# Performance work log

Measured on AMD Instinct MI355X. Metric: run time of the kernel, lower is better.

Reference implementation:

```python
import jax, jax.numpy as jnp
import numpy as np

V, E, H, OUT = 100000, 300, 256, 3
B, LS, LT = 128, 128, 8


def _lstm_scan(xs, Wih, Whh, bih, bhh, reverse):
    # xs: [T, B, E] time-major; returns hidden states [T, B, H] in original time order
    h0 = jnp.zeros((xs.shape[1], H), xs.dtype)
    def step(carry, x):
        h, c = carry
        g = x @ Wih.T + bih + h @ Whh.T + bhh  # [B, 4H]
        i, f, gg, o = jnp.split(g, 4, axis=-1)
        c = jax.nn.sigmoid(f) * c + jax.nn.sigmoid(i) * jnp.tanh(gg)
        h = jax.nn.sigmoid(o) * jnp.tanh(c)
        return (h, c), h
    _, hs = jax.lax.scan(step, (h0, h0), xs, reverse=reverse)
    return hs


def _bidir(emb_bte, Wih_f, Whh_f, bih_f, bhh_f, Wih_b, Whh_b, bih_b, bhh_b):
    xs = jnp.transpose(emb_bte, (1, 0, 2))  # [T, B, E]
    hf = _lstm_scan(xs, Wih_f, Whh_f, bih_f, bhh_f, False)
    hb = _lstm_scan(xs, Wih_b, Whh_b, bih_b, bhh_b, True)
    return jnp.transpose(jnp.concatenate([hf, hb], axis=-1), (1, 0, 2))  # [B, T, 2H]


def setup_inputs() -> dict:
    key = jax.random.key(0)
    ks = jax.random.split(key, 32)
    n = lambda i, shape: 0.05 * jax.random.normal(ks[i], shape, dtype=jnp.float32)
    inp = {
        "sentence_source": jax.random.randint(ks[0], (B, LS), 0, V),
        "target_source": jax.random.randint(ks[1], (B, LT), 0, V),
        "emb_W": n(2, (V, E)),
    }
    names = ["sf", "sb", "tf", "tb"]
    for j, nm in enumerate(names):
        base = 3 + 4 * j
        inp[f"Wih_{nm}"] = n(base + 0, (4 * H, E))
        inp[f"Whh_{nm}"] = n(base + 1, (4 * H, H))
        inp[f"bih_{nm}"] = n(base + 2, (4 * H,))
        inp[f"bhh_{nm}"] = n(base + 3, (4 * H,))
    inp["Wout"] = n(20, (OUT, 2 * H))
    inp["bout"] = n(21, (OUT,))
    return inp


def reference(sentence_source, target_source, emb_W,
              Wih_sf, Whh_sf, bih_sf, bhh_sf,
              Wih_sb, Whh_sb, bih_sb, bhh_sb,
              Wih_tf, Whh_tf, bih_tf, bhh_tf,
              Wih_tb, Whh_tb, bih_tb, bhh_tb,
              Wout, bout):
    emb = emb_W.at[0].set(0.0)  # padding_idx=0
    sen = emb[sentence_source]  # [B, LS, E]  (dropout is identity at eval)
    tgt = emb[target_source]    # [B, LT, E]
    sen_h = _bidir(sen, Wih_sf, Whh_sf, bih_sf, bhh_sf, Wih_sb, Whh_sb, bih_sb, bhh_sb)  # [B, LS, 2H]
    tgt_h = _bidir(tgt, Wih_tf, Whh_tf, bih_tf, bhh_tf, Wih_tb, Whh_tb, bih_tb, bhh_tb)  # [B, LT, 2H]
    A = jnp.einsum("bsh,bth->bst", sen_h, tgt_h)          # [B, LS, LT]
    col = jax.nn.softmax(A, axis=1)
    row = jax.nn.softmax(A, axis=2)
    row_vec = jnp.mean(row, axis=1, keepdims=True)         # [B, 1, LT]
    attn = jnp.einsum("bst,bqt->bsq", col, row_vec)        # [B, LS, 1]
    score = jnp.einsum("bsq,bsh->bqh", attn, sen_h)        # [B, 1, 2H]
    logits = score @ Wout.T + bout                         # [B, 1, OUT]
    return jax.nn.softmax(logits, axis=-1).squeeze()       # [B, OUT]
```

## Files before the change

kernel.cpp:

```cpp
#include <hip/hip_runtime.h>


typedef unsigned short u16;
typedef unsigned long long u64;
typedef float f32x4 __attribute__((ext_vector_type(4)));
typedef int   i32x4 __attribute__((ext_vector_type(4)));
typedef short bf16x8 __attribute__((ext_vector_type(8)));
typedef short s16x4 __attribute__((ext_vector_type(4)));
typedef unsigned short u16x4 __attribute__((ext_vector_type(4)));

#define KP 320
#define KPL 328
#define FH 1024
#define HH 256
#define L2E 1.4426950408889634f

struct Ptr4 { const float* p[4]; };

static __device__ __forceinline__ u16 f2bf(float f) {
    unsigned int u = __float_as_uint(f);
    u += 0x7FFFu + ((u >> 16) & 1u);
    return (u16)(u >> 16);
}
static __device__ __forceinline__ float bf2f(u16 s) {
    return __uint_as_float((unsigned int)s << 16);
}
static __device__ __forceinline__ float sigm2(float x) {
    return __builtin_amdgcn_rcpf(1.0f + __builtin_amdgcn_exp2f(-x));
}
static __device__ __forceinline__ float tanh2(float x) {
    return 1.0f - 2.0f * __builtin_amdgcn_rcpf(1.0f + __builtin_amdgcn_exp2f(x));
}
static __device__ __forceinline__ float tanh_(float x) {
    return 1.0f - 2.0f * __builtin_amdgcn_rcpf(1.0f + __expf(2.0f * x));
}

__global__ __launch_bounds__(256) void pre_kernel(
    const int* __restrict__ sen, const int* __restrict__ tgt,
    const float* __restrict__ emb, Ptr4 Wih, Ptr4 Whh, Ptr4 bih, Ptr4 bhh,
    u16* __restrict__ Xs, u16* __restrict__ Xt,
    u16* __restrict__ WihB, float* __restrict__ biasB,
    char* __restrict__ Wq, float* __restrict__ wdq)
{
    int bid = blockIdx.x, tid = threadIdx.x;
    if (bid < 17408) {
        int row = bid;
        int tok; u16* dst;
        if (row < 16384) { tok = sen[row]; dst = Xs + (size_t)row * KP; }
        else             { tok = tgt[row - 16384]; dst = Xt + (size_t)(row - 16384) * KP; }
        const float* src = emb + (size_t)tok * 300;
        for (int k = tid; k < KP; k += 256) {
            float v = (k < 300 && tok != 0) ? src[k] : 0.0f;
            dst[k] = f2bf(v);
        }
    } else if (bid < 22528) {
        int local = bid - 17408;
        int dir = local / 1280, blk = local - dir * 1280;
        int idx = blk * 256 + tid;
        if (idx < FH * KP) {
            int row = idx / KP, k = idx - row * KP;
            float gsc = ((row >> 8) == 2) ? 2.0f * L2E : L2E;
            WihB[(size_t)dir * FH * KP + idx] =
                (k < 300) ? f2bf(Wih.p[dir][row * 300 + k] * gsc) : (u16)0;
        }
        if (idx < FH) {
            float gsc = ((idx >> 8) == 2) ? 2.0f * L2E : L2E;
            biasB[dir * FH + idx] = (bih.p[dir][idx] + bhh.p[dir][idx]) * gsc;
        }
    } else {
        int local = bid - 22528;
        int w = tid >> 6, lane = tid & 63;
        int pair = local * 4 + w;
        int dir = pair >> 10, row = pair & 1023;
        const float* src = Whh.p[dir] + (size_t)row * HH;
        float m = 0.0f;
        for (int k = lane; k < HH; k += 64) m = fmaxf(m, fabsf(src[k]));
        for (int off = 32; off; off >>= 1) m = fmaxf(m, __shfl_down(m, off));
        m = __shfl(m, 0);
        float qs = (m > 0.0f) ? 127.0f / m : 0.0f;
        char* dst = Wq + (size_t)dir * FH * HH + (size_t)row * HH;
        for (int k = lane; k < HH; k += 64) dst[k] = (char)(int)rintf(src[k] * qs);
        if (lane == 0) {
            float gsc = ((row >> 8) == 2) ? 2.0f * L2E : L2E;
            wdq[dir * FH + row] = (m > 0.0f) ? m / (127.0f * 127.0f) * gsc : 0.0f;
        }
    }
}

__global__ __launch_bounds__(256) void input_gemm_kernel(
    const u16* __restrict__ Xs, const u16* __restrict__ Xt,
    const u16* __restrict__ WihB, const float* __restrict__ biasB,
    u16* __restrict__ Gs, u16* __restrict__ Gt)
{
    __shared__ u16 Bs[64][KPL];

    int bid = blockIdx.x;
    const u16* X; const u16* W; const float* bias; u16* G;
    int lbid, nwg, tsh;
    if (bid < 8192) { lbid = bid;        nwg = 8192; tsh = 7;
                      X = Xs; W = WihB;                         bias = biasB;          G = Gs; }
    else            { lbid = bid - 8192; nwg = 512;  tsh = 3;
                      X = Xt; W = WihB + (size_t)2 * FH * KP;   bias = biasB + 2 * FH; G = Gt; }

    int cpx = nwg >> 3;
    int wid = (lbid & 7) * cpx + (lbid >> 3);
    int nblk = wid & 31;
    int mblk = wid >> 5;
    int dirb = nblk >> 4;
    int u0   = (nblk & 15) * 16;
    size_t dirStride = (size_t)(tsh == 7 ? 16384 : 1024) * FH;

    int tid = threadIdx.x;
    int wave = tid >> 6, lane = tid & 63;
    int r = lane & 15, quad = lane >> 4;
    int m0 = mblk * 64 + wave * 16;

#pragma unroll
    for (int it = 0; it < 10; ++it) {
        int idx = it * 256 + tid;
        int row = idx / 40, cc = idx - row * 40;
        int j = row >> 4, rr = row & 15;
        bf16x8 v = *(const bf16x8*)(W + ((size_t)dirb * FH + j * 256 + u0 + rr) * KP + cc * 8);
        *(bf16x8*)&Bs[row][cc * 8] = v;
    }
    __syncthreads();

    const u16* xr = X + (size_t)(m0 + r) * KP + quad * 8;
    f32x4 acc[4] = {};
#pragma unroll
    for (int k0 = 0; k0 < KP; k0 += 32) {
        bf16x8 a = *(const bf16x8*)(xr + k0);
#pragma unroll
        for (int j = 0; j < 4; ++j) {
            bf16x8 b = *(const bf16x8*)&Bs[j * 16 + r][k0 + quad * 8];
            acc[j] = __builtin_amdgcn_mfma_f32_16x16x32_bf16(a, b, acc[j], 0, 0, 0);
        }
    }

#pragma unroll
    for (int reg = 0; reg < 4; ++reg) {
        int m = m0 + quad * 4 + reg;
        int b = m >> tsh, t = m & ((1 << tsh) - 1);
        int unit = u0 + r;
        u16x4 ov;
#pragma unroll
        for (int j = 0; j < 4; ++j)
            ov[j] = f2bf(acc[j][reg] + bias[dirb * FH + j * 256 + unit]);
        *(u16x4*)(G + (size_t)dirb * dirStride + ((size_t)t * 128 + b) * FH + unit * 4) = ov;
    }
}

__global__ __launch_bounds__(1024, 1) void lstm_scan_kernel(
    const char*  __restrict__ WqB,
    const float* __restrict__ wdq,
    const u16*   __restrict__ Gs,
    const u16*   __restrict__ Gt,
    float* __restrict__ senH,
    float* __restrict__ tgtH)
{
    const int bx  = blockIdx.x;
    const int dir = bx >> 3;
    const int b0  = (bx & 7) << 4;
    const int T   = (dir < 2) ? 128 : 8;
    const int rev = dir & 1;

    const char* Wq = WqB + (size_t)dir * FH * HH;
    const u16*  G  = (dir < 2) ? (Gs + (size_t)dir * 16384 * FH)
                               : (Gt + (size_t)(dir - 2) * 1024 * FH);
    float* Hout = (dir < 2) ? senH : tgtH;
    const int hofs = rev ? 256 : 0;

    const int tid  = threadIdx.x;
    const int w    = tid >> 6, lane = tid & 63;
    const int r    = lane & 15, quad = lane >> 4;
    const int u    = w * 16 + r;

    __shared__ __align__(16) char hb8[2][16][272];

    i32x4 Bq[4][4];
    float dqv[4];
#pragma unroll
    for (int g = 0; g < 4; ++g) {
        int row = g * 256 + u;
        dqv[g] = wdq[dir * FH + row];
#pragma unroll
        for (int kt = 0; kt < 4; ++kt)
            Bq[g][kt] = *(const i32x4*)(Wq + ((size_t)row << 8) + kt * 64 + quad * 16);
    }

    for (int i = tid; i < 2 * 16 * 272; i += 1024) (&hb8[0][0][0])[i] = 0;
    __syncthreads();

    float c[4] = {};
    float hreg[4] = {};
    int tprev = 0;

    s16x4 gvA[4], gvB[4];
    {
        const int t0 = rev ? (T - 1) : 0;
#pragma unroll
        for (int reg = 0; reg < 4; ++reg)
            gvA[reg] = *(const s16x4*)(G + ((size_t)t0 * 128 + b0 + quad * 4 + reg) * FH
                                       + u * 4);
    }

    auto body = [&](int cur, s16x4 (&gvU)[4], s16x4 (&gvP)[4],
                    int t, int tn, int doStore) {
#pragma unroll
        for (int reg = 0; reg < 4; ++reg)
            gvP[reg] = *(const s16x4*)(G + ((size_t)tn * 128 + b0 + quad * 4 + reg) * FH
                                       + u * 4);
        if (doStore) {
#pragma unroll
            for (int reg = 0; reg < 4; ++reg)
                Hout[((size_t)(b0 + quad * 4 + reg) * T + tprev) * 512 + hofs + u]
                    = hreg[reg];
        }

        i32x4 acc[4] = {};
#pragma unroll
        for (int kt = 0; kt < 4; ++kt) {
            i32x4 a = *(const i32x4*)&hb8[cur][r][kt * 64 + quad * 16];
#pragma unroll
            for (int g = 0; g < 4; ++g)
                acc[g] = __builtin_amdgcn_mfma_i32_16x16x64_i8(a, Bq[g][kt], acc[g], 0, 0, 0);
        }

#pragma unroll
        for (int reg = 0; reg < 4; ++reg) {
            int bb = quad * 4 + reg;
            float pi = (float)acc[0][reg] * dqv[0] + bf2f((u16)gvU[reg].x);
            float pf = (float)acc[1][reg] * dqv[1] + bf2f((u16)gvU[reg].y);
            float pg = (float)acc[2][reg] * dqv[2] + bf2f((u16)gvU[reg].z);
            float po = (float)acc[3][reg] * dqv[3] + bf2f((u16)gvU[reg].w);
            float ig = sigm2(pi), fg = sigm2(pf), gg = tanh2(pg), og = sigm2(po);
            float cn = fg * c[reg] + ig * gg;
            c[reg] = cn;
            float hn = og * tanh_(cn);
            hb8[cur ^ 1][bb][u] = (char)(int)rintf(hn * 127.0f);
            hreg[reg] = hn;
        }
        tprev = t;
        __syncthreads();
    };

    for (int s2 = 0; s2 < T; s2 += 2) {
        const int tA = rev ? (T - 1 - s2) : s2;
        const int tB = rev ? (T - 2 - s2) : (s2 + 1);
        const int tC = (s2 + 2 < T) ? (rev ? (T - 3 - s2) : (s2 + 2)) : tB;
        body(0, gvA, gvB, tA, tB, s2 > 0);
        body(1, gvB, gvA, tB, tC, 1);
    }

#pragma unroll
    for (int reg = 0; reg < 4; ++reg)
        Hout[((size_t)(b0 + quad * 4 + reg) * T + tprev) * 512 + hofs + u] = hreg[reg];
}

__global__ __launch_bounds__(256) void attn_out_kernel(
    const float* __restrict__ senH, const float* __restrict__ tgtH,
    const float* __restrict__ Wout, const float* __restrict__ bout,
    float* __restrict__ out)
{
    int b = blockIdx.x, tid = threadIdx.x;
    __shared__ float tg[8][512];
    __shared__ float Am[128][9];
    __shared__ float rowm[128][9];
    __shared__ float mcol[8], csum[8], rvec[8], attn[128], score[512], lg[3];

    const float* tgg = tgtH + (size_t)b * 8 * 512;
    for (int i = tid; i < 4096; i += 256) tg[i >> 9][i & 511] = tgg[i];
    __syncthreads();

    {
        int s = tid >> 1, t0 = (tid & 1) * 4;
        const float* sr = senH + ((size_t)b * 128 + s) * 512;
        float d0 = 0, d1 = 0, d2 = 0, d3 = 0;
        for (int h = 0; h < 512; ++h) {
            float x = sr[h];
            d0 += x * tg[t0 + 0][h]; d1 += x * tg[t0 + 1][h];
            d2 += x * tg[t0 + 2][h]; d3 += x * tg[t0 + 3][h];
        }
        Am[s][t0 + 0] = d0; Am[s][t0 + 1] = d1; Am[s][t0 + 2] = d2; Am[s][t0 + 3] = d3;
    }
    __syncthreads();

    if (tid < 8) {
        float m = -1e30f;
        for (int s = 0; s < 128; ++s) m = fmaxf(m, Am[s][tid]);
        float sum = 0;
        for (int s = 0; s < 128; ++s) sum += __expf(Am[s][tid] - m);
        mcol[tid] = m; csum[tid] = sum;
    }
    if (tid >= 64 && tid < 192) {
        int s = tid - 64;
        float m = -1e30f;
        for (int t = 0; t < 8; ++t) m = fmaxf(m, Am[s][t]);
        float e[8], sum = 0;
        for (int t = 0; t < 8; ++t) { e[t] = __expf(Am[s][t] - m); sum += e[t]; }
        float inv = __builtin_amdgcn_rcpf(sum);
        for (int t = 0; t < 8; ++t) rowm[s][t] = e[t] * inv;
    }
    __syncthreads();
    if (tid < 8) {
        float sum = 0;
        for (int s = 0; s < 128; ++s) sum += rowm[s][tid];
        rvec[tid] = sum * (1.0f / 128.0f);
    }
    __syncthreads();
    if (tid < 128) {
        float a = 0;
        for (int t = 0; t < 8; ++t)
            a += __expf(Am[tid][t] - mcol[t]) / csum[t] * rvec[t];
        attn[tid] = a;
    }
    __syncthreads();
    for (int h = tid; h < 512; h += 256) {
        float acc = 0;
        const float* sp = senH + (size_t)b * 128 * 512 + h;
        for (int s = 0; s < 128; ++s) acc += attn[s] * sp[(size_t)s * 512];
        score[h] = acc;
    }
    __syncthreads();
    if (tid < 3) {
        float acc = bout[tid];
        const float* wr = Wout + tid * 512;
        for (int h = 0; h < 512; ++h) acc += score[h] * wr[h];
        lg[tid] = acc;
    }
    __syncthreads();
    if (tid == 0) {
        float m = fmaxf(lg[0], fmaxf(lg[1], lg[2]));
        float e0 = __expf(lg[0] - m), e1 = __expf(lg[1] - m), e2 = __expf(lg[2] - m);
        float inv = 1.0f / (e0 + e1 + e2);
        out[b * 3 + 0] = e0 * inv; out[b * 3 + 1] = e1 * inv; out[b * 3 + 2] = e2 * inv;
    }
}

extern "C" void kernel_launch(void* const* d_in, const int* in_sizes, int n_in,
                              void* d_out, int out_size, void* d_ws, size_t ws_size,
                              hipStream_t stream)
{
    const int*   sen = (const int*)d_in[0];
    const int*   tgt = (const int*)d_in[1];
    const float* emb = (const float*)d_in[2];
    Ptr4 Wih = {{(const float*)d_in[3],  (const float*)d_in[7],
                 (const float*)d_in[11], (const float*)d_in[15]}};
    Ptr4 Whh = {{(const float*)d_in[4],  (const float*)d_in[8],
                 (const float*)d_in[12], (const float*)d_in[16]}};
    Ptr4 bih = {{(const float*)d_in[5],  (const float*)d_in[9],
                 (const float*)d_in[13], (const float*)d_in[17]}};
    Ptr4 bhh = {{(const float*)d_in[6],  (const float*)d_in[10],
                 (const float*)d_in[14], (const float*)d_in[18]}};
    const float* Wout = (const float*)d_in[19];
    const float* bout = (const float*)d_in[20];
    float* out = (float*)d_out;

    char* ws = (char*)d_ws;
    size_t off = 0;
    auto alloc = [&](size_t bytes) -> void* {
        void* p = ws + off; off += (bytes + 255) & ~(size_t)255; return p;
    };
    u16*   Xs    = (u16*)alloc((size_t)16384 * KP * 2);
    u16*   Xt    = (u16*)alloc((size_t)1024 * KP * 2);
    u16*   WihB  = (u16*)alloc((size_t)4 * FH * KP * 2);
    char*  WqB   = (char*)alloc((size_t)4 * FH * HH);
    float* wdq   = (float*)alloc((size_t)4 * FH * 4);
    float* biasB = (float*)alloc((size_t)4 * FH * 4);
    u16*   Gs    = (u16*)alloc((size_t)2 * 16384 * FH * 2);
    u16*   Gt    = (u16*)alloc((size_t)2 * 1024 * FH * 2);
    float* senH  = (float*)alloc((size_t)128 * 128 * 512 * 4);
    float* tgtH  = (float*)alloc((size_t)128 * 8 * 512 * 4);
    (void)ws_size; (void)in_sizes; (void)n_in; (void)out_size;

    pre_kernel<<<23552, 256, 0, stream>>>(sen, tgt, emb, Wih, Whh, bih, bhh,
                                          Xs, Xt, WihB, biasB, WqB, wdq);
    input_gemm_kernel<<<8704, 256, 0, stream>>>(Xs, Xt, WihB, biasB, Gs, Gt);
    lstm_scan_kernel<<<32, 1024, 0, stream>>>(WqB, wdq, Gs, Gt, senH, tgtH);
    attn_out_kernel<<<128, 256, 0, stream>>>(senH, tgtH, Wout, bout, out);
}
```

Baseline: 577.4 us.

## Double GEMM M-tile, time-major hidden output with pointer stepping, exp2 tanh

The input GEMM now gives each wave 32 rows instead of 16, reusing each B fragment from shared memory for two MFMAs and halving the grid. The LSTM scan writes hidden states in time-major layout [T,B,512] and advances precomputed pointers each step instead of recomputing index arithmetic, and the final tanh uses the exp2-based helper. The attention kernel is updated to read the new layout. This trades more registers per GEMM wave for fewer shared-memory loads and blocks. The strided attention reads may lose some coalescing in exchange for contiguous stores in the scan.

```diff
diff --git a/kernel.cpp b/kernel.cpp
--- a/kernel.cpp
+++ b/kernel.cpp
@@ -30,9 +30,6 @@
 }
 static __device__ __forceinline__ float tanh2(float x) {
     return 1.0f - 2.0f * __builtin_amdgcn_rcpf(1.0f + __builtin_amdgcn_exp2f(x));
-}
-static __device__ __forceinline__ float tanh_(float x) {
-    return 1.0f - 2.0f * __builtin_amdgcn_rcpf(1.0f + __expf(2.0f * x));
 }
 
 __global__ __launch_bounds__(256) void pre_kernel(
@@ -97,9 +94,9 @@
     int bid = blockIdx.x;
     const u16* X; const u16* W; const float* bias; u16* G;
     int lbid, nwg, tsh;
-    if (bid < 8192) { lbid = bid;        nwg = 8192; tsh = 7;
+    if (bid < 4096) { lbid = bid;        nwg = 4096; tsh = 7;
                       X = Xs; W = WihB;                         bias = biasB;          G = Gs; }
-    else            { lbid = bid - 8192; nwg = 512;  tsh = 3;
+    else            { lbid = bid - 4096; nwg = 256;  tsh = 3;
                       X = Xt; W = WihB + (size_t)2 * FH * KP;   bias = biasB + 2 * FH; G = Gt; }
 
     int cpx = nwg >> 3;
@@ -113,7 +110,7 @@
     int tid = threadIdx.x;
     int wave = tid >> 6, lane = tid & 63;
     int r = lane & 15, quad = lane >> 4;
-    int m0 = mblk * 64 + wave * 16;
+    int m0 = mblk * 128 + wave * 32;
 
 #pragma unroll
     for (int it = 0; it < 10; ++it) {
@@ -126,28 +123,32 @@
     __syncthreads();
 
     const u16* xr = X + (size_t)(m0 + r) * KP + quad * 8;
-    f32x4 acc[4] = {};
+    f32x4 acc[2][4] = {};
 #pragma unroll
     for (int k0 = 0; k0 < KP; k0 += 32) {
-        bf16x8 a = *(const bf16x8*)(xr + k0);
+        bf16x8 a0 = *(const bf16x8*)(xr + k0);
+        bf16x8 a1 = *(const bf16x8*)(xr + 16 * KP + k0);
 #pragma unroll
         for (int j = 0; j < 4; ++j) {
             bf16x8 b = *(const bf16x8*)&Bs[j * 16 + r][k0 + quad * 8];
-            acc[j] = __builtin_amdgcn_mfma_f32_16x16x32_bf16(a, b, acc[j], 0, 0, 0);
-        }
-    }
-
-#pragma unroll
-    for (int reg = 0; reg < 4; ++reg) {
-        int m = m0 + quad * 4 + reg;
-        int b = m >> tsh, t = m & ((1 << tsh) - 1);
-        int unit = u0 + r;
-        u16x4 ov;
-#pragma unroll
-        for (int j = 0; j < 4; ++j)
-            ov[j] = f2bf(acc[j][reg] + bias[dirb * FH + j * 256 + unit]);
-        *(u16x4*)(G + (size_t)dirb * dirStride + ((size_t)t * 128 + b) * FH + unit * 4) = ov;
-    }
+            acc[0][j] = __builtin_amdgcn_mfma_f32_16x16x32_bf16(a0, b, acc[0][j], 0, 0, 0);
+            acc[1][j] = __builtin_amdgcn_mfma_f32_16x16x32_bf16(a1, b, acc[1][j], 0, 0, 0);
+        }
+    }
+
+#pragma unroll
+    for (int sub = 0; sub < 2; ++sub)
+#pragma unroll
+        for (int reg = 0; reg < 4; ++reg) {
+            int m = m0 + sub * 16 + quad * 4 + reg;
+            int b = m >> tsh, t = m & ((1 << tsh) - 1);
+            int unit = u0 + r;
+            u16x4 ov;
+#pragma unroll
+            for (int j = 0; j < 4; ++j)
+                ov[j] = f2bf(acc[sub][j][reg] + bias[dirb * FH + j * 256 + unit]);
+            *(u16x4*)(G + (size_t)dirb * dirStride + ((size_t)t * 128 + b) * FH + unit * 4) = ov;
+        }
 }
 
 __global__ __launch_bounds__(1024, 1) void lstm_scan_kernel(
@@ -193,28 +194,32 @@
 
     float c[4] = {};
     float hreg[4] = {};
-    int tprev = 0;
+
+    const int t0 = rev ? (T - 1) : 0;
+    const ptrdiff_t gstep = rev ? -(ptrdiff_t)(128 * FH) : (ptrdiff_t)(128 * FH);
+    const ptrdiff_t hstep = rev ? -(ptrdiff_t)(128 * 512) : (ptrdiff_t)(128 * 512);
+    const u16* gp0 = G + ((size_t)t0 * 128 + b0 + quad * 4) * FH + u * 4;
+    const u16* gp2 = gp0 + 2 * (size_t)FH;
+    float* hp0 = Hout + ((size_t)t0 * 128 + b0 + quad * 4) * 512 + hofs + u;
+    float* hp2 = hp0 + 2 * 512;
 
     s16x4 gvA[4], gvB[4];
-    {
-        const int t0 = rev ? (T - 1) : 0;
-#pragma unroll
-        for (int reg = 0; reg < 4; ++reg)
-            gvA[reg] = *(const s16x4*)(G + ((size_t)t0 * 128 + b0 + quad * 4 + reg) * FH
-                                       + u * 4);
-    }
-
-    auto body = [&](int cur, s16x4 (&gvU)[4], s16x4 (&gvP)[4],
-                    int t, int tn, int doStore) {
-#pragma unroll
-        for (int reg = 0; reg < 4; ++reg)
-            gvP[reg] = *(const s16x4*)(G + ((size_t)tn * 128 + b0 + quad * 4 + reg) * FH
-                                       + u * 4);
+    gvA[0] = *(const s16x4*)(gp0);
+    gvA[1] = *(const s16x4*)(gp0 + FH);
+    gvA[2] = *(const s16x4*)(gp2);
+    gvA[3] = *(const s16x4*)(gp2 + FH);
+    gp0 += gstep; gp2 += gstep;
+
+    auto body = [&](int cur, s16x4 (&gvU)[4], s16x4 (&gvP)[4], int doStore) {
+        gvP[0] = *(const s16x4*)(gp0);
+        gvP[1] = *(const s16x4*)(gp0 + FH);
+        gvP[2] = *(const s16x4*)(gp2);
+        gvP[3] = *(const s16x4*)(gp2 + FH);
+        gp0 += gstep; gp2 += gstep;
         if (doStore) {
-#pragma unroll
-            for (int reg = 0; reg < 4; ++reg)
-                Hout[((size_t)(b0 + quad * 4 + reg) * T + tprev) * 512 + hofs + u]
-                    = hreg[reg];
+            hp0[0] = hreg[0]; hp0[512] = hreg[1];
+            hp2[0] = hreg[2]; hp2[512] = hreg[3];
+            hp0 += hstep; hp2 += hstep;
         }
 
         i32x4 acc[4] = {};
@@ -236,25 +241,20 @@
             float ig = sigm2(pi), fg = sigm2(pf), gg = tanh2(pg), og = sigm2(po);
             float cn = fg * c[reg] + ig * gg;
             c[reg] = cn;
-            float hn = og * tanh_(cn);
+            float hn = og * tanh2(cn * (2.0f * L2E));
             hb8[cur ^ 1][bb][u] = (char)(int)rintf(hn * 127.0f);
             hreg[reg] = hn;
         }
-        tprev = t;
         __syncthreads();
     };
 
     for (int s2 = 0; s2 < T; s2 += 2) {
-        const int tA = rev ? (T - 1 - s2) : s2;
-        const int tB = rev ? (T - 2 - s2) : (s2 + 1);
-        const int tC = (s2 + 2 < T) ? (rev ? (T - 3 - s2) : (s2 + 2)) : tB;
-        body(0, gvA, gvB, tA, tB, s2 > 0);
-        body(1, gvB, gvA, tB, tC, 1);
-    }
-
-#pragma unroll
-    for (int reg = 0; reg < 4; ++reg)
-        Hout[((size_t)(b0 + quad * 4 + reg) * T + tprev) * 512 + hofs + u] = hreg[reg];
+        body(0, gvA, gvB, s2 > 0);
+        body(1, gvB, gvA, 1);
+    }
+
+    hp0[0] = hreg[0]; hp0[512] = hreg[1];
+    hp2[0] = hreg[2]; hp2[512] = hreg[3];
 }
 
 __global__ __launch_bounds__(256) void attn_out_kernel(
@@ -268,13 +268,15 @@
     __shared__ float rowm[128][9];
     __shared__ float mcol[8], csum[8], rvec[8], attn[128], score[512], lg[3];
 
-    const float* tgg = tgtH + (size_t)b * 8 * 512;
-    for (int i = tid; i < 4096; i += 256) tg[i >> 9][i & 511] = tgg[i];
+    for (int i = tid; i < 4096; i += 256) {
+        int t = i >> 9, h = i & 511;
+        tg[t][h] = tgtH[((size_t)t * 128 + b) * 512 + h];
+    }
     __syncthreads();
 
     {
         int s = tid >> 1, t0 = (tid & 1) * 4;
-        const float* sr = senH + ((size_t)b * 128 + s) * 512;
+        const float* sr = senH + ((size_t)s * 128 + b) * 512;
         float d0 = 0, d1 = 0, d2 = 0, d3 = 0;
         for (int h = 0; h < 512; ++h) {
             float x = sr[h];
@@ -317,8 +319,8 @@
     __syncthreads();
     for (int h = tid; h < 512; h += 256) {
         float acc = 0;
-        const float* sp = senH + (size_t)b * 128 * 512 + h;
-        for (int s = 0; s < 128; ++s) acc += attn[s] * sp[(size_t)s * 512];
+        const float* sp = senH + b * 512 + h;
+        for (int s = 0; s < 128; ++s) acc += attn[s] * sp[(size_t)s * 128 * 512];
         score[h] = acc;
     }
     __syncthreads();
@@ -375,7 +377,7 @@
 
     pre_kernel<<<23552, 256, 0, stream>>>(sen, tgt, emb, Wih, Whh, bih, bhh,
                                           Xs, Xt, WihB, biasB, WqB, wdq);
-    input_gemm_kernel<<<8704, 256, 0, stream>>>(Xs, Xt, WihB, biasB, Gs, Gt);
+    input_gemm_kernel<<<4352, 256, 0, stream>>>(Xs, Xt, WihB, biasB, Gs, Gt);
     lstm_scan_kernel<<<32, 1024, 0, stream>>>(WqB, wdq, Gs, Gt, senH, tgtH);
     attn_out_kernel<<<128, 256, 0, stream>>>(senH, tgtH, Wout, bout, out);
 }
```

After: 503.9 us. -12.7%, faster.
